# Optimization experiments

Hardware: AMD Instinct MI355X
Metric: run time of the kernel (lower is better)

## Reference

```python
import jax, jax.numpy as jnp
import numpy as np

N = 50000      # nodes
E = 800000     # edges
IN = 128       # in_channels
HID = 128      # hidden_channels
OUT = 2        # out_channels (edge classes)
HEADS = 8      # EGConv default num_heads
BASES = 4      # EGConv default num_bases
FH = HID // HEADS  # per-head feature dim = 16


def _egconv(x, Wb, Wc, bc, b, row, col, norm, n):
    """One EGConv layer (aggregators=['symnorm']), self-loops already in row/col/norm.
    Wb: [in, BASES*FH] basis projection (no bias).
    Wc: [in, HEADS*BASES], bc: combination weights linear.
    b : [HID] output bias.
    """
    bases = x @ Wb                                            # [n, BASES*FH]
    msg = bases[row] * norm[:, None]                          # gather + symnorm scale
    agg = jax.ops.segment_sum(msg, col, num_segments=n)       # scatter-add -> [n, BASES*FH]
    w = (x @ Wc + bc).reshape(n, HEADS, BASES)                # per-node combination weights
    out = jnp.einsum('nhb,nbf->nhf', w, agg.reshape(n, BASES, FH))
    return out.reshape(n, HEADS * FH) + b


def setup_inputs() -> dict:
    key = jax.random.key(0)
    ks = jax.random.split(key, 12)
    s = 0.05
    inp = {
        'x': jax.random.normal(ks[0], (N, IN), jnp.float32),
        'edge_index': jax.random.randint(ks[1], (2, E), 0, N, jnp.int64),
        # conv1
        'Wb1': jax.random.normal(ks[2], (IN, BASES * FH), jnp.float32) * s,
        'Wc1': jax.random.normal(ks[3], (IN, HEADS * BASES), jnp.float32) * s,
        'bc1': jnp.zeros((HEADS * BASES,), jnp.float32),
        'b1': jnp.zeros((HID,), jnp.float32),
        # conv2
        'Wb2': jax.random.normal(ks[4], (HID, BASES * FH), jnp.float32) * s,
        'Wc2': jax.random.normal(ks[5], (HID, HEADS * BASES), jnp.float32) * s,
        'bc2': jnp.zeros((HEADS * BASES,), jnp.float32),
        'b2': jnp.zeros((HID,), jnp.float32),
        # edge classifier
        'Wcls': jax.random.normal(ks[6], (2 * HID, OUT), jnp.float32) * s,
        'bcls': jnp.zeros((OUT,), jnp.float32),
    }
    return inp


def reference(x, edge_index, Wb1, Wc1, bc1, b1, Wb2, Wc2, bc2, b2, Wcls, bcls):
    n = x.shape[0]
    # add self loops (EGConv default add_self_loops=True) + gcn_norm symnorm weights
    sl = jnp.arange(n, dtype=edge_index.dtype)
    row = jnp.concatenate([edge_index[0], sl])
    col = jnp.concatenate([edge_index[1], sl])
    deg = jax.ops.segment_sum(jnp.ones(row.shape[0], x.dtype), col, num_segments=n)
    dis = jnp.where(deg > 0, deg, 1.0) ** -0.5
    dis = jnp.where(deg > 0, dis, 0.0)
    norm = dis[row] * dis[col]                                # symnorm edge weight

    h = jax.nn.relu(_egconv(x, Wb1, Wc1, bc1, b1, row, col, norm, n))
    h = _egconv(h, Wb2, Wc2, bc2, b2, row, col, norm, n)

    # edge classifier: gather endpoint embeddings of ORIGINAL edges, concat, linear
    e = jnp.concatenate([h[edge_index[0]], h[edge_index[1]]], axis=-1)  # [E, 2*HID]
    return e @ Wcls + bcls
```

## Files before the change

### kernel.cpp

```cpp
#include <hip/hip_runtime.h>
#include <hip/hip_fp16.h>

#define NN 50000
#define EE 800000
#define NB_E2 1563
#define NB_CNT 782
#define NWIN 2
#define WIN 25000
#define EPB 1024
#define NCHUNK 782

__global__ void k_count(const int* __restrict__ ei, int* cnt, unsigned* __restrict__ pk) {
    int t = blockIdx.x * 256 + threadIdx.x;
    int base = t * 4;
    if (base + 3 < EE) {
        int4 cc = *(const int4*)(ei + EE + base);
        unsigned r0 = (unsigned)atomicAdd(&cnt[cc.x], 1);
        unsigned r1 = (unsigned)atomicAdd(&cnt[cc.y], 1);
        unsigned r2 = (unsigned)atomicAdd(&cnt[cc.z], 1);
        unsigned r3 = (unsigned)atomicAdd(&cnt[cc.w], 1);
        *(uint4*)(pk + base) = make_uint4((unsigned)cc.x | (r0 << 16),
                                          (unsigned)cc.y | (r1 << 16),
                                          (unsigned)cc.z | (r2 << 16),
                                          (unsigned)cc.w | (r3 << 16));
    } else {
        for (int e = 0; e < 4; e++) {
            int tt = base + e;
            if (tt < EE) {
                int c = ei[EE + tt];
                unsigned r = (unsigned)atomicAdd(&cnt[c], 1);
                pk[tt] = (unsigned)c | (r << 16);
            }
        }
    }
}

__global__ void k_scan(const int* __restrict__ cnt, float* __restrict__ dis,
                       int2* __restrict__ sd, int* __restrict__ starts, int n) {
    __shared__ int s[256];
    int tid = threadIdx.x, b = blockIdx.x;
    int i = b * 256 + tid;
    int v = (i < n) ? cnt[i] : 0;
    if (i < n) dis[i] = rsqrtf((float)v + 1.0f);
    s[tid] = v;
    __syncthreads();
    for (int off = 1; off < 256; off <<= 1) {
        int t2 = (tid >= off) ? s[tid - off] : 0;
        __syncthreads();
        if (tid >= off) s[tid] += t2;
        __syncthreads();
    }
    int loc = s[tid] - v;
    int lim = b * 256;
    int pre = 0;
    for (int j = tid * 4; j < lim; j += 1024) {
        int4 c4 = *(const int4*)(cnt + j);
        pre += c4.x + c4.y + c4.z + c4.w;
    }
    __syncthreads();
    s[tid] = pre;
    __syncthreads();
    for (int off = 128; off; off >>= 1) {
        if (tid < off) s[tid] += s[tid + off];
        __syncthreads();
    }
    int boff = s[0];
    if (i < n) {
        int st = loc + boff;
        sd[i] = make_int2(st, v);
        starts[i] = st;
    }
}

__global__ __launch_bounds__(256) void k_fill(
    const int* __restrict__ ei, const unsigned* __restrict__ pk,
    const int* __restrict__ starts, int* __restrict__ csr)
{
    int w = blockIdx.x & (NWIN - 1);
    int chunk = blockIdx.x >> 1;
    int base = chunk * EPB + threadIdx.x * 4;
    unsigned lo = w * WIN, hi = lo + WIN;
    if (base + 3 < EE) {
        int4 rr = *(const int4*)(ei + base);
        uint4 pp = *(const uint4*)(pk + base);
        unsigned c0 = pp.x & 0xffffu, c1 = pp.y & 0xffffu;
        unsigned c2 = pp.z & 0xffffu, c3 = pp.w & 0xffffu;
        if (c0 >= lo && c0 < hi) csr[starts[c0] + (pp.x >> 16)] = rr.x;
        if (c1 >= lo && c1 < hi) csr[starts[c1] + (pp.y >> 16)] = rr.y;
        if (c2 >= lo && c2 < hi) csr[starts[c2] + (pp.z >> 16)] = rr.z;
        if (c3 >= lo && c3 < hi) csr[starts[c3] + (pp.w >> 16)] = rr.w;
    } else {
        for (int e = 0; e < 4; e++) {
            int t = base + e;
            if (t < EE) {
                unsigned pv = pk[t];
                unsigned c = pv & 0xffffu;
                if (c >= lo && c < hi) csr[starts[c] + (pv >> 16)] = ei[t];
            }
        }
    }
}

__global__ __launch_bounds__(256) void k_gemm(
    const float* __restrict__ x, const float* __restrict__ Wb,
    const float* __restrict__ Wc, const float* __restrict__ bc,
    const float* __restrict__ dis,
    __half* __restrict__ bsh, float* __restrict__ wcomb, int n)
{
    __shared__ float xt[32 * 257];
    int tid = threadIdx.x;
    int grp = blockIdx.y;
    int row0 = blockIdx.x * 256;
    int row = row0 + tid;
    bool valid = row < n;

    const float* W = (grp < 2) ? (Wb + grp * 32) : Wc;
    const int ldw = (grp < 2) ? 64 : 32;

    float acc[32];
#pragma unroll
    for (int c = 0; c < 32; c++) acc[c] = 0.f;

    for (int s = 0; s < 4; s++) {
        int base_k = s * 32;
        float4 v[8];
#pragma unroll
        for (int i = 0; i < 8; i++) {
            int idx = i * 256 + tid;
            int r = idx >> 3;
            int k4 = idx & 7;
            int gr = row0 + r;
            v[i] = (gr < n) ? *(const float4*)(x + (size_t)gr * 128 + base_k + k4 * 4)
                            : make_float4(0.f, 0.f, 0.f, 0.f);
        }
        __syncthreads();
#pragma unroll
        for (int i = 0; i < 8; i++) {
            int idx = i * 256 + tid;
            int r = idx >> 3;
            int k4 = idx & 7;
            xt[(k4 * 4 + 0) * 257 + r] = v[i].x;
            xt[(k4 * 4 + 1) * 257 + r] = v[i].y;
            xt[(k4 * 4 + 2) * 257 + r] = v[i].z;
            xt[(k4 * 4 + 3) * 257 + r] = v[i].w;
        }
        __syncthreads();

        const float* Ws = W + base_k * ldw;
#pragma unroll 8
        for (int k = 0; k < 32; k++) {
            float xs = xt[k * 257 + tid];
            const float* wk = Ws + k * ldw;
#pragma unroll
            for (int c = 0; c < 32; c++) acc[c] = fmaf(xs, wk[c], acc[c]);
        }
    }

    if (!valid) return;
    if (grp < 2) {
        float d = dis[row];
        __half2 hh[16];
#pragma unroll
        for (int c = 0; c < 16; c++)
            hh[c] = __floats2half2_rn(acc[2 * c] * d, acc[2 * c + 1] * d);
        uint4* bo = (uint4*)(bsh + (size_t)row * 64 + grp * 32);
        const uint4* src = (const uint4*)hh;
#pragma unroll
        for (int c = 0; c < 4; c++) bo[c] = src[c];
    } else {
        float4* wo = (float4*)(wcomb + (size_t)row * 32);
#pragma unroll
        for (int c = 0; c < 8; c++)
            wo[c] = make_float4(acc[4*c] + bc[4*c], acc[4*c+1] + bc[4*c+1],
                                acc[4*c+2] + bc[4*c+2], acc[4*c+3] + bc[4*c+3]);
    }
}

template<int LAYER2>
__global__ __launch_bounds__(256) void k_agg(
    const int* __restrict__ csr, const int2* __restrict__ sd,
    const __half* __restrict__ bsh, const float* __restrict__ dis,
    const float* __restrict__ wcomb, const float* __restrict__ bias,
    float* __restrict__ h,
    const float* __restrict__ Wcls, const float* __restrict__ bcls,
    float* __restrict__ p, int n)
{
    int wid = (blockIdx.x * 256 + threadIdx.x) >> 6;
    int lane = threadIdx.x & 63;
    if (wid >= n) return;
    int2 s2 = sd[wid];
    int start = s2.x, deg = s2.y;
    int g = lane >> 4, q = lane & 15;

    const uint2* bsp = (const uint2*)bsh;
    float4 acc4 = make_float4(0.f, 0.f, 0.f, 0.f);
    if (g == 0) {
        uint2 v = bsp[(size_t)wid * 16 + q];
        float2 lo = __half22float2(*(const __half2*)&v.x);
        float2 hi = __half22float2(*(const __half2*)&v.y);
        acc4 = make_float4(lo.x, lo.y, hi.x, hi.y);
    }

    int j = 0;
    int ia = 0, ib = 0;
    if (8 <= deg) { ia = csr[start + g]; ib = csr[start + 4 + g]; }
    while (j + 8 <= deg) {
        int jn = j + 8;
        int na = 0, nb = 0;
        if (jn + 8 <= deg) { na = csr[start + jn + g]; nb = csr[start + jn + 4 + g]; }
        uint2 v0 = bsp[(size_t)ia * 16 + q];
        uint2 v1 = bsp[(size_t)ib * 16 + q];
        float2 l0 = __half22float2(*(const __half2*)&v0.x);
        float2 h0 = __half22float2(*(const __half2*)&v0.y);
        float2 l1 = __half22float2(*(const __half2*)&v1.x);
        float2 h1 = __half22float2(*(const __half2*)&v1.y);
        acc4.x += l0.x + l1.x;
        acc4.y += l0.y + l1.y;
        acc4.z += h0.x + h1.x;
        acc4.w += h0.y + h1.y;
        ia = na; ib = nb; j = jn;
    }
    int last = start + deg - 1;
    for (; j < deg; j += 4) {
        int idx = start + j + g;
        int r = csr[min(idx, last)];
        uint2 v = bsp[(size_t)r * 16 + q];
        float2 lo = __half22float2(*(const __half2*)&v.x);
        float2 hi = __half22float2(*(const __half2*)&v.y);
        float m = (j + g < deg) ? 1.f : 0.f;
        acc4.x = fmaf(lo.x, m, acc4.x);
        acc4.y = fmaf(lo.y, m, acc4.y);
        acc4.z = fmaf(hi.x, m, acc4.z);
        acc4.w = fmaf(hi.y, m, acc4.w);
    }

    acc4.x += __shfl_xor(acc4.x, 16, 64);
    acc4.y += __shfl_xor(acc4.y, 16, 64);
    acc4.z += __shfl_xor(acc4.z, 16, 64);
    acc4.w += __shfl_xor(acc4.w, 16, 64);
    acc4.x += __shfl_xor(acc4.x, 32, 64);
    acc4.y += __shfl_xor(acc4.y, 32, 64);
    acc4.z += __shfl_xor(acc4.z, 32, 64);
    acc4.w += __shfl_xor(acc4.w, 32, 64);

    float d = dis[wid];
    acc4.x *= d; acc4.y *= d; acc4.z *= d; acc4.w *= d;

    int src = lane >> 2;
    float t0 = __shfl(acc4.x, src, 64);
    float t1 = __shfl(acc4.y, src, 64);
    float t2 = __shfl(acc4.z, src, 64);
    float t3 = __shfl(acc4.w, src, 64);
    int c = lane & 3;
    float acc = (c == 0) ? t0 : (c == 1) ? t1 : (c == 2) ? t2 : t3;

    int fh = lane & 15;
    float a0 = __shfl(acc, fh, 64);
    float a1 = __shfl(acc, 16 + fh, 64);
    float a2 = __shfl(acc, 32 + fh, 64);
    float a3 = __shfl(acc, 48 + fh, 64);
    const float* wn = wcomb + (size_t)wid * 32;
    int hd = lane >> 4;
    float s1 = bias[lane];
    float s2v = bias[64 + lane];
    s1 = fmaf(wn[hd * 4 + 0], a0, s1);
    s1 = fmaf(wn[hd * 4 + 1], a1, s1);
    s1 = fmaf(wn[hd * 4 + 2], a2, s1);
    s1 = fmaf(wn[hd * 4 + 3], a3, s1);
    s2v = fmaf(wn[(4 + hd) * 4 + 0], a0, s2v);
    s2v = fmaf(wn[(4 + hd) * 4 + 1], a1, s2v);
    s2v = fmaf(wn[(4 + hd) * 4 + 2], a2, s2v);
    s2v = fmaf(wn[(4 + hd) * 4 + 3], a3, s2v);

    if (!LAYER2) {
        s1 = fmaxf(s1, 0.f);
        s2v = fmaxf(s2v, 0.f);
        h[(size_t)wid * 128 + lane] = s1;
        h[(size_t)wid * 128 + 64 + lane] = s2v;
    } else {
        float r0 = s1 * Wcls[lane * 2 + 0] + s2v * Wcls[(64 + lane) * 2 + 0];
        float r1 = s1 * Wcls[lane * 2 + 1] + s2v * Wcls[(64 + lane) * 2 + 1];
        float r2 = s1 * Wcls[(128 + lane) * 2 + 0] + s2v * Wcls[(192 + lane) * 2 + 0];
        float r3 = s1 * Wcls[(128 + lane) * 2 + 1] + s2v * Wcls[(192 + lane) * 2 + 1];
#pragma unroll
        for (int off = 32; off; off >>= 1) {
            r0 += __shfl_xor(r0, off, 64);
            r1 += __shfl_xor(r1, off, 64);
            r2 += __shfl_xor(r2, off, 64);
            r3 += __shfl_xor(r3, off, 64);
        }
        if (lane == 0) {
            p[wid * 4 + 0] = r0 + bcls[0];
            p[wid * 4 + 1] = r1 + bcls[1];
            p[wid * 4 + 2] = r2;
            p[wid * 4 + 3] = r3;
        }
    }
}

__global__ void k_edge(const int* __restrict__ ei, const float* __restrict__ p,
                       float* __restrict__ out)
{
    int t = blockIdx.x * blockDim.x + threadIdx.x;
    if (t >= EE / 2) return;
    int2 rr = *(const int2*)(ei + 2 * t);
    int2 cc = *(const int2*)(ei + EE + 2 * t);
    float2 pt0 = *(const float2*)(p + rr.x * 4);
    float2 pt1 = *(const float2*)(p + rr.y * 4);
    float2 pb0 = *(const float2*)(p + cc.x * 4 + 2);
    float2 pb1 = *(const float2*)(p + cc.y * 4 + 2);
    float4 o;
    o.x = pt0.x + pb0.x;
    o.y = pt0.y + pb0.y;
    o.z = pt1.x + pb1.x;
    o.w = pt1.y + pb1.y;
    *(float4*)(out + (size_t)t * 4) = o;
}

extern "C" void kernel_launch(void* const* d_in, const int* in_sizes, int n_in,
                              void* d_out, int out_size, void* d_ws, size_t ws_size,
                              hipStream_t stream) {
    const float* x    = (const float*)d_in[0];
    const int*   ei   = (const int*)d_in[1];
    const float* Wb1  = (const float*)d_in[2];
    const float* Wc1  = (const float*)d_in[3];
    const float* bc1  = (const float*)d_in[4];
    const float* b1   = (const float*)d_in[5];
    const float* Wb2  = (const float*)d_in[6];
    const float* Wc2  = (const float*)d_in[7];
    const float* bc2  = (const float*)d_in[8];
    const float* b2   = (const float*)d_in[9];
    const float* Wcls = (const float*)d_in[10];
    const float* bcls = (const float*)d_in[11];
    float* out = (float*)d_out;

    char* ws = (char*)d_ws;
    size_t off = 0;
    auto alloc = [&](size_t bytes) {
        void* pp = ws + off;
        off += (bytes + 15) & ~(size_t)15;
        return pp;
    };

    float*    dis    = (float*)alloc(50048 * 4);
    __half*   bsh    = (__half*)alloc((size_t)NN * 64 * 2);
    float*    wcomb  = (float*)alloc((size_t)NN * 32 * 4);
    float*    h      = (float*)alloc((size_t)NN * 128 * 4);
    float*    p      = (float*)alloc((size_t)NN * 4 * 4);
    int*      cnt    = (int*)alloc(50048 * 4);
    int*      starts = (int*)alloc(50048 * 4);
    int2*     sd     = (int2*)alloc((size_t)50048 * 8);
    int*      csr    = (int*)alloc((size_t)EE * 4);
    unsigned* pk     = (unsigned*)alloc((size_t)EE * 4);

    const int B = 256;
    int gN   = (NN + B - 1) / B;
    int gN64 = (NN * 64) / B;
    dim3 gG(gN, 3);

    hipMemsetAsync(cnt, 0, NN * sizeof(int), stream);
    k_count<<<NB_CNT, B, 0, stream>>>(ei, cnt, pk);
    k_scan<<<gN, B, 0, stream>>>(cnt, dis, sd, starts, NN);
    k_fill<<<NCHUNK * NWIN, B, 0, stream>>>(ei, pk, starts, csr);

    k_gemm<<<gG, B, 0, stream>>>(x, Wb1, Wc1, bc1, dis, bsh, wcomb, NN);
    k_agg<0><<<gN64, B, 0, stream>>>(csr, sd, bsh, dis, wcomb, b1, h,
                                     Wcls, bcls, p, NN);

    k_gemm<<<gG, B, 0, stream>>>(h, Wb2, Wc2, bc2, dis, bsh, wcomb, NN);
    k_agg<1><<<gN64, B, 0, stream>>>(csr, sd, bsh, dis, wcomb, b2, h,
                                     Wcls, bcls, p, NN);

    k_edge<<<NB_E2, B, 0, stream>>>(ei, p, out);
}
```

Before: 280.6 us.

## Build CSR with per-chunk LDS histograms instead of global atomics

```diff
diff --git a/kernel.cpp b/kernel.cpp
--- a/kernel.cpp
+++ b/kernel.cpp
@@ -2,46 +2,74 @@
 #include <hip/hip_fp16.h>
 
 #define NN 50000
+#define NNP 50048
 #define EE 800000
+#define CH 32
+#define CHE (EE / CH)
 #define NB_E2 1563
-#define NB_CNT 782
-#define NWIN 2
-#define WIN 25000
+#define NWIN 4
+#define WIN 12500
 #define EPB 1024
 #define NCHUNK 782
 
-__global__ void k_count(const int* __restrict__ ei, int* cnt, unsigned* __restrict__ pk) {
-    int t = blockIdx.x * 256 + threadIdx.x;
-    int base = t * 4;
-    if (base + 3 < EE) {
-        int4 cc = *(const int4*)(ei + EE + base);
-        unsigned r0 = (unsigned)atomicAdd(&cnt[cc.x], 1);
-        unsigned r1 = (unsigned)atomicAdd(&cnt[cc.y], 1);
-        unsigned r2 = (unsigned)atomicAdd(&cnt[cc.z], 1);
-        unsigned r3 = (unsigned)atomicAdd(&cnt[cc.w], 1);
-        *(uint4*)(pk + base) = make_uint4((unsigned)cc.x | (r0 << 16),
-                                          (unsigned)cc.y | (r1 << 16),
-                                          (unsigned)cc.z | (r2 << 16),
-                                          (unsigned)cc.w | (r3 << 16));
-    } else {
-        for (int e = 0; e < 4; e++) {
-            int tt = base + e;
-            if (tt < EE) {
-                int c = ei[EE + tt];
-                unsigned r = (unsigned)atomicAdd(&cnt[c], 1);
-                pk[tt] = (unsigned)c | (r << 16);
-            }
-        }
-    }
-}
-
-__global__ void k_scan(const int* __restrict__ cnt, float* __restrict__ dis,
-                       int2* __restrict__ sd, int* __restrict__ starts, int n) {
+__global__ __launch_bounds__(256) void k_count(
+    const int* __restrict__ ei, unsigned* __restrict__ pk, int* __restrict__ part)
+{
+    __shared__ int hist[WIN];
+    int c = blockIdx.x >> 2;
+    int w = blockIdx.x & 3;
+    int tid = threadIdx.x;
+    for (int i = tid; i < WIN; i += 256) hist[i] = 0;
+    __syncthreads();
+    int e0 = c * CHE;
+    unsigned lo = w * WIN;
+    const int* cols = ei + EE + e0;
+    for (int i = tid; i < CHE / 4; i += 256) {
+        int4 cc = *(const int4*)(cols + i * 4);
+        unsigned d;
+        d = (unsigned)cc.x - lo;
+        if (d < WIN) {
+            int r = atomicAdd(&hist[d], 1);
+            pk[e0 + i * 4 + 0] = (unsigned)cc.x | ((unsigned)c << 16) | ((unsigned)r << 21);
+        }
+        d = (unsigned)cc.y - lo;
+        if (d < WIN) {
+            int r = atomicAdd(&hist[d], 1);
+            pk[e0 + i * 4 + 1] = (unsigned)cc.y | ((unsigned)c << 16) | ((unsigned)r << 21);
+        }
+        d = (unsigned)cc.z - lo;
+        if (d < WIN) {
+            int r = atomicAdd(&hist[d], 1);
+            pk[e0 + i * 4 + 2] = (unsigned)cc.z | ((unsigned)c << 16) | ((unsigned)r << 21);
+        }
+        d = (unsigned)cc.w - lo;
+        if (d < WIN) {
+            int r = atomicAdd(&hist[d], 1);
+            pk[e0 + i * 4 + 3] = (unsigned)cc.w | ((unsigned)c << 16) | ((unsigned)r << 21);
+        }
+    }
+    __syncthreads();
+    int* pc = part + (size_t)c * NNP + lo;
+    for (int i = tid; i < WIN; i += 256) pc[i] = hist[i];
+}
+
+__global__ void k_reduce(const int* __restrict__ part, int* __restrict__ cnt,
+                         float* __restrict__ dis) {
+    int i = blockIdx.x * 256 + threadIdx.x;
+    if (i >= NN) return;
+    int v = 0;
+#pragma unroll
+    for (int c = 0; c < CH; c++) v += part[(size_t)c * NNP + i];
+    cnt[i] = v;
+    dis[i] = rsqrtf((float)v + 1.0f);
+}
+
+__global__ void k_scan(const int* __restrict__ cnt, const int* __restrict__ part,
+                       int2* __restrict__ sd, int* __restrict__ chunkstart, int n) {
     __shared__ int s[256];
     int tid = threadIdx.x, b = blockIdx.x;
     int i = b * 256 + tid;
     int v = (i < n) ? cnt[i] : 0;
-    if (i < n) dis[i] = rsqrtf((float)v + 1.0f);
     s[tid] = v;
     __syncthreads();
     for (int off = 1; off < 256; off <<= 1) {
@@ -68,34 +96,40 @@
     if (i < n) {
         int st = loc + boff;
         sd[i] = make_int2(st, v);
-        starts[i] = st;
+        int cs = st;
+#pragma unroll
+        for (int c = 0; c < CH; c++) {
+            chunkstart[(size_t)c * NNP + i] = cs;
+            cs += part[(size_t)c * NNP + i];
+        }
     }
 }
 
 __global__ __launch_bounds__(256) void k_fill(
     const int* __restrict__ ei, const unsigned* __restrict__ pk,
-    const int* __restrict__ starts, int* __restrict__ csr)
+    const int* __restrict__ chunkstart, int* __restrict__ csr)
 {
     int w = blockIdx.x & (NWIN - 1);
-    int chunk = blockIdx.x >> 1;
+    int chunk = blockIdx.x >> 2;
     int base = chunk * EPB + threadIdx.x * 4;
-    unsigned lo = w * WIN, hi = lo + WIN;
+    unsigned lo = w * WIN;
     if (base + 3 < EE) {
         int4 rr = *(const int4*)(ei + base);
         uint4 pp = *(const uint4*)(pk + base);
         unsigned c0 = pp.x & 0xffffu, c1 = pp.y & 0xffffu;
         unsigned c2 = pp.z & 0xffffu, c3 = pp.w & 0xffffu;
-        if (c0 >= lo && c0 < hi) csr[starts[c0] + (pp.x >> 16)] = rr.x;
-        if (c1 >= lo && c1 < hi) csr[starts[c1] + (pp.y >> 16)] = rr.y;
-        if (c2 >= lo && c2 < hi) csr[starts[c2] + (pp.z >> 16)] = rr.z;
-        if (c3 >= lo && c3 < hi) csr[starts[c3] + (pp.w >> 16)] = rr.w;
+        if (c0 - lo < WIN) csr[chunkstart[(size_t)((pp.x >> 16) & 31u) * NNP + c0] + (pp.x >> 21)] = rr.x;
+        if (c1 - lo < WIN) csr[chunkstart[(size_t)((pp.y >> 16) & 31u) * NNP + c1] + (pp.y >> 21)] = rr.y;
+        if (c2 - lo < WIN) csr[chunkstart[(size_t)((pp.z >> 16) & 31u) * NNP + c2] + (pp.z >> 21)] = rr.z;
+        if (c3 - lo < WIN) csr[chunkstart[(size_t)((pp.w >> 16) & 31u) * NNP + c3] + (pp.w >> 21)] = rr.w;
     } else {
         for (int e = 0; e < 4; e++) {
             int t = base + e;
             if (t < EE) {
                 unsigned pv = pk[t];
-                unsigned c = pv & 0xffffu;
-                if (c >= lo && c < hi) csr[starts[c] + (pv >> 16)] = ei[t];
+                unsigned cgl = pv & 0xffffu;
+                if (cgl - lo < WIN)
+                    csr[chunkstart[(size_t)((pv >> 16) & 31u) * NNP + cgl] + (pv >> 21)] = ei[t];
             }
         }
     }
@@ -348,20 +382,21 @@
     float*    h      = (float*)alloc((size_t)NN * 128 * 4);
     float*    p      = (float*)alloc((size_t)NN * 4 * 4);
     int*      cnt    = (int*)alloc(50048 * 4);
-    int*      starts = (int*)alloc(50048 * 4);
     int2*     sd     = (int2*)alloc((size_t)50048 * 8);
     int*      csr    = (int*)alloc((size_t)EE * 4);
     unsigned* pk     = (unsigned*)alloc((size_t)EE * 4);
+    int*      part   = (int*)alloc((size_t)CH * NNP * 4);
+    int*      chunkstart = (int*)alloc((size_t)CH * NNP * 4);
 
     const int B = 256;
     int gN   = (NN + B - 1) / B;
     int gN64 = (NN * 64) / B;
     dim3 gG(gN, 3);
 
-    hipMemsetAsync(cnt, 0, NN * sizeof(int), stream);
-    k_count<<<NB_CNT, B, 0, stream>>>(ei, cnt, pk);
-    k_scan<<<gN, B, 0, stream>>>(cnt, dis, sd, starts, NN);
-    k_fill<<<NCHUNK * NWIN, B, 0, stream>>>(ei, pk, starts, csr);
+    k_count<<<CH * NWIN, B, 0, stream>>>(ei, pk, part);
+    k_reduce<<<gN, B, 0, stream>>>(part, cnt, dis);
+    k_scan<<<gN, B, 0, stream>>>(cnt, part, sd, chunkstart, NN);
+    k_fill<<<NCHUNK * NWIN, B, 0, stream>>>(ei, pk, chunkstart, csr);
 
     k_gemm<<<gG, B, 0, stream>>>(x, Wb1, Wc1, bc1, dis, bsh, wcomb, NN);
     k_agg<0><<<gN64, B, 0, stream>>>(csr, sd, bsh, dis, wcomb, b1, h,
```

Result: faster. 265.6 us (-5.3%).
